# Optimization experiments

Measured on AMD Instinct MI355X. Metric: run time of the kernel, lower is better.

Reference implementation:

```python
import jax, jax.numpy as jnp
import numpy as np

B, F, N_COMP, DEGREE = 8192, 4096, 512, 3
GAMMA = 1.0  # coef0 = 0.0 -> no bias column


def setup_inputs() -> dict:
    key = jax.random.key(0)
    k1, k2, k3 = jax.random.split(key, 3)
    X = jax.random.normal(k1, (B, F), dtype=jnp.float32)
    index_hash = jax.random.randint(k2, (DEGREE, F), 0, N_COMP, dtype=jnp.int32)
    bit_hash = jax.random.randint(k3, (DEGREE, F), 0, 2, dtype=jnp.int32)  # 0/1 -> mapped to +-1
    return {"X": X, "index_hash": index_hash, "bit_hash": bit_hash}


def reference(X, index_hash, bit_hash):
    # CountSketch per degree + TensorSketch product via rFFT.
    sgn = (bit_hash * 2 - 1).astype(X.dtype)          # [D, F] in {-1, +1}
    X_ext = X * (GAMMA ** 0.5)                        # [B, F]

    def count_sketch(idx_d, sgn_d):
        # scatter-add hashed, signed features into N_COMP buckets (per batch row)
        vals = X_ext * sgn_d                          # [B, F]
        return jnp.zeros((X.shape[0], N_COMP), X.dtype).at[:, idx_d].add(vals)

    sketches = jax.vmap(count_sketch)(index_hash, sgn)  # [D, B, N]
    Fr = jnp.fft.rfft(sketches, axis=-1)                # [D, B, N//2+1]
    prod = jnp.prod(Fr, axis=0)                         # [B, N//2+1]
    return jnp.fft.irfft(prod, n=N_COMP, axis=-1)       # [B, N]
```

## Files before the change

kernel.cpp:

```cpp
#include <hip/hip_runtime.h>
#include <math.h>


#define F_DIM 4096
#define NC 512
#define DEG 3
#define THREADS 256
#define PI_F 3.14159265358979323846f

#define OFS_STRIDE 520
#define ENT_BYTE_OFF 4096

__device__ __forceinline__ float2 cmul(float2 a, float2 b) {
    return make_float2(a.x * b.x - a.y * b.y, a.x * b.y + a.y * b.x);
}
__device__ __forceinline__ float2 cmulc(float2 a, float2 b) {
    return make_float2(a.x * b.x + a.y * b.y, a.y * b.x - a.x * b.y);
}
__device__ __forceinline__ float2 shflx(float2 v, int m) {
    return make_float2(__shfl_xor(v.x, m), __shfl_xor(v.y, m));
}

__device__ __forceinline__ void fwd_lane_stage(float2 (&s)[8], int lane, int m, float2 w) {
    const bool up = (lane & m) != 0;
    const float sg = up ? -1.0f : 1.0f;
    const float2 weff = up ? w : make_float2(1.0f, 0.0f);
    #pragma unroll
    for (int r = 0; r < 8; ++r) {
        const float2 zz = s[r];
        const float2 pp = shflx(zz, m);
        const float2 dd = make_float2(fmaf(sg, zz.x, pp.x), fmaf(sg, zz.y, pp.y));
        s[r] = cmul(dd, weff);
    }
}
__device__ __forceinline__ void inv_lane_stage(float2 (&s)[8], int lane, int m, float2 w) {
    const bool up = (lane & m) != 0;
    const float sg = up ? -1.0f : 1.0f;
    #pragma unroll
    for (int r = 0; r < 8; ++r) {
        const float2 zz = s[r];
        const float2 pp = shflx(zz, m);
        const float2 a  = up ? pp : zz;
        const float2 bs = up ? zz : pp;
        const float2 t  = cmulc(bs, w);
        s[r] = make_float2(fmaf(sg, t.x, a.x), fmaf(sg, t.y, a.y));
    }
}

__global__ __launch_bounds__(512) void build_csr(
    const int* __restrict__ idxh,
    const int* __restrict__ bith,
    ushort* __restrict__ ofs_g,
    ushort* __restrict__ ent_g)
{
    __shared__ unsigned cnt[NC];
    __shared__ unsigned scn[NC];
    const int d = blockIdx.x;
    const int t = threadIdx.x;

    if (t < NC) cnt[t] = 0;
    __syncthreads();
    for (int f = t; f < F_DIM; f += 512)
        atomicAdd(&cnt[idxh[d * F_DIM + f]], 1u);
    __syncthreads();

    if (t < NC) scn[t] = cnt[t];
    __syncthreads();
    for (int off = 1; off < NC; off <<= 1) {
        unsigned v = 0;
        if (t < NC) { v = scn[t]; if (t >= off) v += scn[t - off]; }
        __syncthreads();
        if (t < NC) scn[t] = v;
        __syncthreads();
    }

    if (t < NC) {
        const unsigned excl = t ? scn[t - 1] : 0u;
        ofs_g[d * OFS_STRIDE + t] = (ushort)excl;
        cnt[t] = excl;
    }
    if (t == 0) ofs_g[d * OFS_STRIDE + NC] = (ushort)F_DIM;
    __syncthreads();

    for (int f = t; f < F_DIM; f += 512) {
        const int b = idxh[d * F_DIM + f];
        const unsigned pos = atomicAdd(&cnt[b], 1u);
        ent_g[d * F_DIM + pos] = (ushort)(f | (bith[d * F_DIM + f] << 15));
    }
}

__global__ __launch_bounds__(THREADS, 3) void ts_kernel(
    const float* __restrict__ X,
    const ushort* __restrict__ ofs_g,
    const ushort* __restrict__ ent_g,
    float* __restrict__ out)
{
    __shared__ float4 xst4[F_DIM / 2];
    __shared__ float2 exch[DEG][NC];
    float2* xst = (float2*)xst4;

    const int tid  = threadIdx.x;
    const int lane = tid & 63;
    const int wave = tid >> 6;

    int je0[DEG][2], je1[DEG][2];
    #pragma unroll
    for (int d = 0; d < DEG; ++d)
        #pragma unroll
        for (int h = 0; h < 2; ++h) {
            const int b = tid + (h << 8);
            je0[d][h] = ofs_g[d * OFS_STRIDE + b];
            je1[d][h] = ofs_g[d * OFS_STRIDE + b + 1];
        }

    const float wang = -2.0f * PI_F / 512.0f;
    float2 tw0[4], tw1[2], tw2, tw3, tw4, tw5, tw6, tw7;
    #pragma unroll
    for (int c = 0; c < 4; ++c) {
        float sv, cv; __sincosf(wang * (float)(c * 64 + lane), &sv, &cv);
        tw0[c] = make_float2(cv, sv);
    }
    #pragma unroll
    for (int c = 0; c < 2; ++c) {
        float sv, cv; __sincosf(wang * (float)(2 * (c * 64 + lane)), &sv, &cv);
        tw1[c] = make_float2(cv, sv);
    }
    { float sv, cv; __sincosf(wang * (float)(4 * lane),          &sv, &cv); tw2 = make_float2(cv, sv); }
    { float sv, cv; __sincosf(wang * (float)(8 * (lane & 31)),   &sv, &cv); tw3 = make_float2(cv, sv); }
    { float sv, cv; __sincosf(wang * (float)(16 * (lane & 15)),  &sv, &cv); tw4 = make_float2(cv, sv); }
    { float sv, cv; __sincosf(wang * (float)(32 * (lane & 7)),   &sv, &cv); tw5 = make_float2(cv, sv); }
    { float sv, cv; __sincosf(wang * (float)(64 * (lane & 3)),   &sv, &cv); tw6 = make_float2(cv, sv); }
    { float sv, cv; __sincosf(wang * (float)(128 * (lane & 1)),  &sv, &cv); tw7 = make_float2(cv, sv); }

    int jp0 = 0;
    if (lane >= 1) { const int msb = 31 - __builtin_clz((unsigned)lane); jp0 = lane ^ ((1 << msb) - 1); }

    float2 z[DEG][8];

    for (int p = 0; p < 4; ++p) {
        const int pr0 = blockIdx.x * 8 + p * 2;
        const float4* X0q = (const float4*)(X + (size_t)pr0 * F_DIM);
        const float4* X1q = (const float4*)(X + (size_t)(pr0 + 1) * F_DIM);
        #pragma unroll
        for (int k = 0; k < 4; ++k) {
            const int i4 = tid + k * THREADS;
            const float4 a = X0q[i4];
            const float4 b = X1q[i4];
            xst4[2 * i4]     = make_float4(a.x, b.x, a.y, b.y);
            xst4[2 * i4 + 1] = make_float4(a.z, b.z, a.w, b.w);
        }
        __syncthreads();

        #pragma unroll
        for (int d = 0; d < DEG; ++d)
            #pragma unroll
            for (int h = 0; h < 2; ++h) {
                const int b = tid + (h << 8);
                const ushort* ep = ent_g + d * F_DIM;
                float ax = 0.0f, ay = 0.0f;
                int e = je0[d][h];
                const int eend = je1[d][h];
                for (; e + 4 <= eend; e += 4) {
                    const ushort u0 = ep[e], u1 = ep[e + 1], u2 = ep[e + 2], u3 = ep[e + 3];
                    const float2 v0 = xst[u0 & 4095], v1 = xst[u1 & 4095];
                    const float2 v2 = xst[u2 & 4095], v3 = xst[u3 & 4095];
                    const float s0 = (u0 & 0x8000) ? 1.0f : -1.0f;
                    const float s1 = (u1 & 0x8000) ? 1.0f : -1.0f;
                    const float s2 = (u2 & 0x8000) ? 1.0f : -1.0f;
                    const float s3 = (u3 & 0x8000) ? 1.0f : -1.0f;
                    ax += s0 * v0.x + s1 * v1.x + s2 * v2.x + s3 * v3.x;
                    ay += s0 * v0.y + s1 * v1.y + s2 * v2.y + s3 * v3.y;
                }
                for (; e < eend; ++e) {
                    const ushort u = ep[e];
                    const float2 v = xst[u & 4095];
                    const float s = (u & 0x8000) ? 1.0f : -1.0f;
                    ax += s * v.x; ay += s * v.y;
                }
                exch[d][b] = make_float2(ax, ay);
            }
        __syncthreads();

        if (wave == p) {
            #pragma unroll
            for (int d = 0; d < DEG; ++d)
                #pragma unroll
                for (int it = 0; it < 8; ++it)
                    z[d][it] = exch[d][it * 64 + lane];
        }
        __syncthreads();
    }

    float2 P0[8], P1[8];
    #pragma unroll
    for (int it = 0; it < 8; ++it) { P0[it] = make_float2(1.0f, 0.0f); P1[it] = make_float2(1.0f, 0.0f); }

    #pragma unroll
    for (int d = 0; d < DEG; ++d) {
        float2 s[8];
        #pragma unroll
        for (int it = 0; it < 8; ++it) s[it] = z[d][it];

        #pragma unroll
        for (int c = 0; c < 4; ++c) {
            const float2 a = s[c], b = s[c + 4];
            s[c]     = make_float2(a.x + b.x, a.y + b.y);
            s[c + 4] = cmul(make_float2(a.x - b.x, a.y - b.y), tw0[c]);
        }
        #pragma unroll
        for (int g = 0; g < 2; ++g)
            #pragma unroll
            for (int c = 0; c < 2; ++c) {
                const int i1 = g * 4 + c, i2 = i1 + 2;
                const float2 a = s[i1], b = s[i2];
                s[i1] = make_float2(a.x + b.x, a.y + b.y);
                s[i2] = cmul(make_float2(a.x - b.x, a.y - b.y), tw1[c]);
            }
        #pragma unroll
        for (int g = 0; g < 4; ++g) {
            const int i1 = 2 * g, i2 = i1 + 1;
            const float2 a = s[i1], b = s[i2];
            s[i1] = make_float2(a.x + b.x, a.y + b.y);
            s[i2] = cmul(make_float2(a.x - b.x, a.y - b.y), tw2);
        }
        fwd_lane_stage(s, lane, 32, tw3);
        fwd_lane_stage(s, lane, 16, tw4);
        fwd_lane_stage(s, lane, 8,  tw5);
        fwd_lane_stage(s, lane, 4,  tw6);
        fwd_lane_stage(s, lane, 2,  tw7);
        fwd_lane_stage(s, lane, 1,  make_float2(1.0f, 0.0f));

        float2 zp[8];
        zp[0] = make_float2(__shfl(s[0].x, jp0), __shfl(s[0].y, jp0));
        zp[1] = shflx(s[1], 63);
        zp[2] = shflx(s[3], 63);
        zp[3] = shflx(s[2], 63);
        zp[4] = shflx(s[7], 63);
        zp[5] = shflx(s[6], 63);
        zp[6] = shflx(s[5], 63);
        zp[7] = shflx(s[4], 63);
        #pragma unroll
        for (int it = 0; it < 8; ++it) {
            const float2 zk = s[it], zq = zp[it];
            const float2 A = make_float2(0.5f * (zk.x + zq.x), 0.5f * (zk.y - zq.y));
            const float2 B = make_float2(0.5f * (zk.y + zq.y), 0.5f * (zq.x - zk.x));
            P0[it] = cmul(P0[it], A);
            P1[it] = cmul(P1[it], B);
        }
    }

    float2 q[8];
    #pragma unroll
    for (int it = 0; it < 8; ++it)
        q[it] = make_float2(P0[it].x - P1[it].y, P0[it].y + P1[it].x);

    inv_lane_stage(q, lane, 1,  make_float2(1.0f, 0.0f));
    inv_lane_stage(q, lane, 2,  tw7);
    inv_lane_stage(q, lane, 4,  tw6);
    inv_lane_stage(q, lane, 8,  tw5);
    inv_lane_stage(q, lane, 16, tw4);
    inv_lane_stage(q, lane, 32, tw3);
    #pragma unroll
    for (int g = 0; g < 4; ++g) {
        const int i1 = 2 * g, i2 = i1 + 1;
        const float2 a = q[i1];
        const float2 t = cmulc(q[i2], tw2);
        q[i1] = make_float2(a.x + t.x, a.y + t.y);
        q[i2] = make_float2(a.x - t.x, a.y - t.y);
    }
    #pragma unroll
    for (int g = 0; g < 2; ++g)
        #pragma unroll
        for (int c = 0; c < 2; ++c) {
            const int i1 = g * 4 + c, i2 = i1 + 2;
            const float2 a = q[i1];
            const float2 t = cmulc(q[i2], tw1[c]);
            q[i1] = make_float2(a.x + t.x, a.y + t.y);
            q[i2] = make_float2(a.x - t.x, a.y - t.y);
        }
    #pragma unroll
    for (int c = 0; c < 4; ++c) {
        const float2 a = q[c];
        const float2 t = cmulc(q[c + 4], tw0[c]);
        q[c]     = make_float2(a.x + t.x, a.y + t.y);
        q[c + 4] = make_float2(a.x - t.x, a.y - t.y);
    }

    const float scale = 1.0f / (float)NC;
    const int r0 = blockIdx.x * 8 + wave * 2;
    float* o0 = out + (size_t)r0 * NC;
    float* o1 = o0 + NC;
    #pragma unroll
    for (int it = 0; it < 8; ++it) {
        const int n = it * 64 + lane;
        o0[n] = q[it].x * scale;
        o1[n] = q[it].y * scale;
    }
}

extern "C" void kernel_launch(void* const* d_in, const int* in_sizes, int n_in,
                              void* d_out, int out_size, void* d_ws, size_t ws_size,
                              hipStream_t stream) {
    const float* X    = (const float*)d_in[0];
    const int*   idxh = (const int*)d_in[1];
    const int*   bith = (const int*)d_in[2];
    float*       outp = (float*)d_out;

    ushort* ofs_g = (ushort*)d_ws;
    ushort* ent_g = (ushort*)((char*)d_ws + ENT_BYTE_OFF);

    build_csr<<<DEG, 512, 0, stream>>>(idxh, bith, ofs_g, ent_g);

    const int n_rows = in_sizes[0] / F_DIM;
    const int blocks = n_rows / 8;
    ts_kernel<<<blocks, THREADS, 0, stream>>>(X, ofs_g, ent_g, outp);
}
```

Before: 263.2 us.

## Split feature dimension into quarters with per-wave private LDS tiles

```diff
diff --git a/kernel.cpp b/kernel.cpp
--- a/kernel.cpp
+++ b/kernel.cpp
@@ -8,8 +8,10 @@
 #define THREADS 256
 #define PI_F 3.14159265358979323846f
 
-#define OFS_STRIDE 520
-#define ENT_BYTE_OFF 4096
+#define NQ 4
+#define QF (F_DIM / NQ)
+#define OFSQ_STRIDE 513
+#define ENT_BYTE_OFF 16384
 
 __device__ __forceinline__ float2 cmul(float2 a, float2 b) {
     return make_float2(a.x * b.x - a.y * b.y, a.x * b.y + a.y * b.x);
@@ -50,68 +52,104 @@
 __global__ __launch_bounds__(512) void build_csr(
     const int* __restrict__ idxh,
     const int* __restrict__ bith,
-    ushort* __restrict__ ofs_g,
+    ushort* __restrict__ ofsq_g,
     ushort* __restrict__ ent_g)
 {
     __shared__ unsigned cnt[NC];
     __shared__ unsigned scn[NC];
-    const int d = blockIdx.x;
+    const int d = blockIdx.x >> 2;
+    const int q = blockIdx.x & 3;
     const int t = threadIdx.x;
-
-    if (t < NC) cnt[t] = 0;
-    __syncthreads();
-    for (int f = t; f < F_DIM; f += 512)
-        atomicAdd(&cnt[idxh[d * F_DIM + f]], 1u);
-    __syncthreads();
-
-    if (t < NC) scn[t] = cnt[t];
+    const int fbase = d * F_DIM + q * QF;
+
+    cnt[t] = 0;
+    __syncthreads();
+    for (int f = t; f < QF; f += 512)
+        atomicAdd(&cnt[idxh[fbase + f]], 1u);
+    __syncthreads();
+
+    scn[t] = cnt[t];
     __syncthreads();
     for (int off = 1; off < NC; off <<= 1) {
-        unsigned v = 0;
-        if (t < NC) { v = scn[t]; if (t >= off) v += scn[t - off]; }
+        unsigned v = scn[t];
+        if (t >= off) v += scn[t - off];
         __syncthreads();
-        if (t < NC) scn[t] = v;
+        scn[t] = v;
         __syncthreads();
     }
 
-    if (t < NC) {
-        const unsigned excl = t ? scn[t - 1] : 0u;
-        ofs_g[d * OFS_STRIDE + t] = (ushort)excl;
-        cnt[t] = excl;
-    }
-    if (t == 0) ofs_g[d * OFS_STRIDE + NC] = (ushort)F_DIM;
-    __syncthreads();
-
-    for (int f = t; f < F_DIM; f += 512) {
-        const int b = idxh[d * F_DIM + f];
+    const unsigned excl = t ? scn[t - 1] : 0u;
+    ofsq_g[blockIdx.x * OFSQ_STRIDE + t] = (ushort)excl;
+    cnt[t] = excl;
+    if (t == 0) ofsq_g[blockIdx.x * OFSQ_STRIDE + NC] = (ushort)QF;
+    __syncthreads();
+
+    for (int f = t; f < QF; f += 512) {
+        const int b = idxh[fbase + f];
         const unsigned pos = atomicAdd(&cnt[b], 1u);
-        ent_g[d * F_DIM + pos] = (ushort)(f | (bith[d * F_DIM + f] << 15));
-    }
-}
-
-__global__ __launch_bounds__(THREADS, 3) void ts_kernel(
+        ent_g[blockIdx.x * QF + pos] = (ushort)(f | (bith[fbase + f] << 15));
+    }
+}
+
+__global__ __launch_bounds__(THREADS, 4) void ts_kernel(
     const float* __restrict__ X,
-    const ushort* __restrict__ ofs_g,
+    const ushort* __restrict__ ofsq_g,
     const ushort* __restrict__ ent_g,
     float* __restrict__ out)
 {
-    __shared__ float4 xst4[F_DIM / 2];
-    __shared__ float2 exch[DEG][NC];
-    float2* xst = (float2*)xst4;
+    __shared__ float2 xst[4][QF];
 
     const int tid  = threadIdx.x;
     const int lane = tid & 63;
     const int wave = tid >> 6;
-
-    int je0[DEG][2], je1[DEG][2];
+    const int pair = blockIdx.x * 4 + wave;
+    const int r0   = pair * 2;
+
+    float2* xw = xst[wave];
+    float4* xw4 = (float4*)xw;
+
+    float2 z[DEG][8];
     #pragma unroll
     for (int d = 0; d < DEG; ++d)
         #pragma unroll
-        for (int h = 0; h < 2; ++h) {
-            const int b = tid + (h << 8);
-            je0[d][h] = ofs_g[d * OFS_STRIDE + b];
-            je1[d][h] = ofs_g[d * OFS_STRIDE + b + 1];
-        }
+        for (int it = 0; it < 8; ++it)
+            z[d][it] = make_float2(0.0f, 0.0f);
+
+    for (int q = 0; q < NQ; ++q) {
+        const float4* X0q = (const float4*)(X + (size_t)r0 * F_DIM + q * QF);
+        const float4* X1q = (const float4*)(X + (size_t)(r0 + 1) * F_DIM + q * QF);
+        #pragma unroll
+        for (int k = 0; k < 4; ++k) {
+            const int i4 = lane + k * 64;
+            const float4 a = X0q[i4];
+            const float4 b = X1q[i4];
+            xw4[2 * i4]     = make_float4(a.x, b.x, a.y, b.y);
+            xw4[2 * i4 + 1] = make_float4(a.z, b.z, a.w, b.w);
+        }
+
+        #pragma unroll
+        for (int d = 0; d < DEG; ++d) {
+            const int blkq = d * NQ + q;
+            const ushort* ofs = ofsq_g + blkq * OFSQ_STRIDE;
+            const ushort* ep  = ent_g + blkq * QF;
+            #pragma unroll
+            for (int it = 0; it < 8; ++it) {
+                const int b = it * 64 + lane;
+                int e = ofs[b];
+                const int eend = ofs[b + 1];
+                float ax = 0.0f, ay = 0.0f;
+                for (; e < eend; ++e) {
+                    const ushort u = ep[e];
+                    const float2 v = xw[u & 1023];
+                    const float s = (u & 0x8000) ? 1.0f : -1.0f;
+                    ax += s * v.x;
+                    ay += s * v.y;
+                }
+                z[d][it].x += ax;
+                z[d][it].y += ay;
+            }
+        }
+    }
 
     const float wang = -2.0f * PI_F / 512.0f;
     float2 tw0[4], tw1[2], tw2, tw3, tw4, tw5, tw6, tw7;
@@ -134,62 +172,6 @@
 
     int jp0 = 0;
     if (lane >= 1) { const int msb = 31 - __builtin_clz((unsigned)lane); jp0 = lane ^ ((1 << msb) - 1); }
-
-    float2 z[DEG][8];
-
-    for (int p = 0; p < 4; ++p) {
-        const int pr0 = blockIdx.x * 8 + p * 2;
-        const float4* X0q = (const float4*)(X + (size_t)pr0 * F_DIM);
-        const float4* X1q = (const float4*)(X + (size_t)(pr0 + 1) * F_DIM);
-        #pragma unroll
-        for (int k = 0; k < 4; ++k) {
-            const int i4 = tid + k * THREADS;
-            const float4 a = X0q[i4];
-            const float4 b = X1q[i4];
-            xst4[2 * i4]     = make_float4(a.x, b.x, a.y, b.y);
-            xst4[2 * i4 + 1] = make_float4(a.z, b.z, a.w, b.w);
-        }
-        __syncthreads();
-
-        #pragma unroll
-        for (int d = 0; d < DEG; ++d)
-            #pragma unroll
-            for (int h = 0; h < 2; ++h) {
-                const int b = tid + (h << 8);
-                const ushort* ep = ent_g + d * F_DIM;
-                float ax = 0.0f, ay = 0.0f;
-                int e = je0[d][h];
-                const int eend = je1[d][h];
-                for (; e + 4 <= eend; e += 4) {
-                    const ushort u0 = ep[e], u1 = ep[e + 1], u2 = ep[e + 2], u3 = ep[e + 3];
-                    const float2 v0 = xst[u0 & 4095], v1 = xst[u1 & 4095];
-                    const float2 v2 = xst[u2 & 4095], v3 = xst[u3 & 4095];
-                    const float s0 = (u0 & 0x8000) ? 1.0f : -1.0f;
-                    const float s1 = (u1 & 0x8000) ? 1.0f : -1.0f;
-                    const float s2 = (u2 & 0x8000) ? 1.0f : -1.0f;
-                    const float s3 = (u3 & 0x8000) ? 1.0f : -1.0f;
-                    ax += s0 * v0.x + s1 * v1.x + s2 * v2.x + s3 * v3.x;
-                    ay += s0 * v0.y + s1 * v1.y + s2 * v2.y + s3 * v3.y;
-                }
-                for (; e < eend; ++e) {
-                    const ushort u = ep[e];
-                    const float2 v = xst[u & 4095];
-                    const float s = (u & 0x8000) ? 1.0f : -1.0f;
-                    ax += s * v.x; ay += s * v.y;
-                }
-                exch[d][b] = make_float2(ax, ay);
-            }
-        __syncthreads();
-
-        if (wave == p) {
-            #pragma unroll
-            for (int d = 0; d < DEG; ++d)
-                #pragma unroll
-                for (int it = 0; it < 8; ++it)
-                    z[d][it] = exch[d][it * 64 + lane];
-        }
-        __syncthreads();
-    }
 
     float2 P0[8], P1[8];
     #pragma unroll
@@ -249,52 +231,51 @@
         }
     }
 
-    float2 q[8];
+    float2 q2[8];
     #pragma unroll
     for (int it = 0; it < 8; ++it)
-        q[it] = make_float2(P0[it].x - P1[it].y, P0[it].y + P1[it].x);
-
-    inv_lane_stage(q, lane, 1,  make_float2(1.0f, 0.0f));
-    inv_lane_stage(q, lane, 2,  tw7);
-    inv_lane_stage(q, lane, 4,  tw6);
-    inv_lane_stage(q, lane, 8,  tw5);
-    inv_lane_stage(q, lane, 16, tw4);
-    inv_lane_stage(q, lane, 32, tw3);
+        q2[it] = make_float2(P0[it].x - P1[it].y, P0[it].y + P1[it].x);
+
+    inv_lane_stage(q2, lane, 1,  make_float2(1.0f, 0.0f));
+    inv_lane_stage(q2, lane, 2,  tw7);
+    inv_lane_stage(q2, lane, 4,  tw6);
+    inv_lane_stage(q2, lane, 8,  tw5);
+    inv_lane_stage(q2, lane, 16, tw4);
+    inv_lane_stage(q2, lane, 32, tw3);
     #pragma unroll
     for (int g = 0; g < 4; ++g) {
         const int i1 = 2 * g, i2 = i1 + 1;
-        const float2 a = q[i1];
-        const float2 t = cmulc(q[i2], tw2);
-        q[i1] = make_float2(a.x + t.x, a.y + t.y);
-        q[i2] = make_float2(a.x - t.x, a.y - t.y);
+        const float2 a = q2[i1];
+        const float2 t = cmulc(q2[i2], tw2);
+        q2[i1] = make_float2(a.x + t.x, a.y + t.y);
+        q2[i2] = make_float2(a.x - t.x, a.y - t.y);
     }
     #pragma unroll
     for (int g = 0; g < 2; ++g)
         #pragma unroll
         for (int c = 0; c < 2; ++c) {
             const int i1 = g * 4 + c, i2 = i1 + 2;
-            const float2 a = q[i1];
-            const float2 t = cmulc(q[i2], tw1[c]);
-            q[i1] = make_float2(a.x + t.x, a.y + t.y);
-            q[i2] = make_float2(a.x - t.x, a.y - t.y);
+            const float2 a = q2[i1];
+            const float2 t = cmulc(q2[i2], tw1[c]);
+            q2[i1] = make_float2(a.x + t.x, a.y + t.y);
+            q2[i2] = make_float2(a.x - t.x, a.y - t.y);
         }
     #pragma unroll
     for (int c = 0; c < 4; ++c) {
-        const float2 a = q[c];
-        const float2 t = cmulc(q[c + 4], tw0[c]);
-        q[c]     = make_float2(a.x + t.x, a.y + t.y);
-        q[c + 4] = make_float2(a.x - t.x, a.y - t.y);
+        const float2 a = q2[c];
+        const float2 t = cmulc(q2[c + 4], tw0[c]);
+        q2[c]     = make_float2(a.x + t.x, a.y + t.y);
+        q2[c + 4] = make_float2(a.x - t.x, a.y - t.y);
     }
 
     const float scale = 1.0f / (float)NC;
-    const int r0 = blockIdx.x * 8 + wave * 2;
     float* o0 = out + (size_t)r0 * NC;
     float* o1 = o0 + NC;
     #pragma unroll
     for (int it = 0; it < 8; ++it) {
         const int n = it * 64 + lane;
-        o0[n] = q[it].x * scale;
-        o1[n] = q[it].y * scale;
+        o0[n] = q2[it].x * scale;
+        o1[n] = q2[it].y * scale;
     }
 }
 
@@ -306,12 +287,12 @@
     const int*   bith = (const int*)d_in[2];
     float*       outp = (float*)d_out;
 
-    ushort* ofs_g = (ushort*)d_ws;
-    ushort* ent_g = (ushort*)((char*)d_ws + ENT_BYTE_OFF);
-
-    build_csr<<<DEG, 512, 0, stream>>>(idxh, bith, ofs_g, ent_g);
+    ushort* ofsq_g = (ushort*)d_ws;
+    ushort* ent_g  = (ushort*)((char*)d_ws + ENT_BYTE_OFF);
+
+    build_csr<<<DEG * NQ, 512, 0, stream>>>(idxh, bith, ofsq_g, ent_g);
 
     const int n_rows = in_sizes[0] / F_DIM;
     const int blocks = n_rows / 8;
-    ts_kernel<<<blocks, THREADS, 0, stream>>>(X, ofs_g, ent_g, outp);
-}
+    ts_kernel<<<blocks, THREADS, 0, stream>>>(X, ofsq_g, ent_g, outp);
+}
```

After: 296.5 us. 12.6% more time.
